# Kernel tuning notes

Hardware: AMD Instinct MI355X
Metric: run time of the kernel (lower is better)

Reference implementation:

```python
import jax, jax.numpy as jnp
import numpy as np

D_MODEL = 1024
NUM_HEADS = 16
DEPTH = D_MODEL // NUM_HEADS
B, S = 4, 2048


def setup_inputs() -> dict:
    key = jax.random.key(0)
    ks = jax.random.split(key, 13)
    sd = 1.0 / np.sqrt(D_MODEL)
    inp = {
        "q_in": jax.random.normal(ks[0], (B, S, D_MODEL), jnp.float32),
        "k_in": jax.random.normal(ks[1], (B, S, D_MODEL), jnp.float32),
        "v_in": jax.random.normal(ks[2], (B, S, D_MODEL), jnp.float32),
        # binary padding/causal-style mask: 1 = masked position
        "m_in": (jax.random.uniform(ks[3], (B, 1, S, S)) < 0.1).astype(jnp.float32),
        "Wq": jax.random.normal(ks[4], (D_MODEL, D_MODEL), jnp.float32) * sd,
        "bq": jax.random.normal(ks[5], (D_MODEL,), jnp.float32) * 0.01,
        "Wk": jax.random.normal(ks[6], (D_MODEL, D_MODEL), jnp.float32) * sd,
        "bk": jax.random.normal(ks[7], (D_MODEL,), jnp.float32) * 0.01,
        "Wv": jax.random.normal(ks[8], (D_MODEL, D_MODEL), jnp.float32) * sd,
        "bv": jax.random.normal(ks[9], (D_MODEL,), jnp.float32) * 0.01,
        "Wo": jax.random.normal(ks[10], (D_MODEL, D_MODEL), jnp.float32) * sd,
        "bo": jax.random.normal(ks[11], (D_MODEL,), jnp.float32) * 0.01,
    }
    return inp


def _split(t):
    # [B,S,D] -> [B,H,S,depth]
    b, s, _ = t.shape
    return t.reshape(b, s, NUM_HEADS, DEPTH).transpose(0, 2, 1, 3)


def reference(q_in, k_in, v_in, m_in, Wq, bq, Wk, bk, Wv, bv, Wo, bo):
    # torch Linear: x @ W^T + b
    q = _split(q_in @ Wq.T + bq)
    k = _split(k_in @ Wk.T + bk)
    v = _split(v_in @ Wv.T + bv)
    scale = jnp.sqrt(jnp.asarray(DEPTH, jnp.float32))
    scores = jnp.einsum("bhqd,bhkd->bhqk", q, k) / scale
    scores = scores - m_in * 1e6
    attn = jax.nn.softmax(scores, axis=-1)
    out = jnp.einsum("bhqk,bhkd->bhqd", attn, v)  # [B,H,S,depth]
    out = out.transpose(0, 2, 1, 3).reshape(q_in.shape[0], -1, D_MODEL)
    return out @ Wo.T + bo
```

## Files before the change

kernel.cpp:

```cpp
#include <hip/hip_runtime.h>


typedef __bf16 bf16_t;
typedef __bf16 bf16x4 __attribute__((ext_vector_type(4)));
typedef __bf16 bf16x8 __attribute__((ext_vector_type(8)));
typedef float floatx2 __attribute__((ext_vector_type(2)));
typedef float floatx4 __attribute__((ext_vector_type(4)));
typedef float floatx16 __attribute__((ext_vector_type(16)));

#define DMODEL 1024
#define NHEAD  16
#define DEPTH  64
#define BATCH  4
#define SEQ    2048
#define MROWS  (BATCH * SEQ)

#define QSCALE 0.18033688011112042f

#define GLDS16(gaddr, laddr)                                                   \
  __builtin_amdgcn_global_load_lds(                                            \
      (__attribute__((address_space(1))) void*)(gaddr),                        \
      (__attribute__((address_space(3))) void*)(laddr), 16, 0, 0)

__global__ __launch_bounds__(256) void cvt_weights(
    const float* __restrict__ w0, const float* __restrict__ w1,
    const float* __restrict__ w2, const float* __restrict__ w3,
    bf16_t* __restrict__ out) {
  const int n_per4 = (DMODEL * DMODEL) / 4;
  int idx = blockIdx.x * blockDim.x + threadIdx.x;
  int t = idx / n_per4;
  int e4 = idx - t * n_per4;
  const float* src = (t == 0) ? w0 : (t == 1) ? w1 : (t == 2) ? w2 : w3;
  const float sc = (t == 0) ? QSCALE : 1.0f;
  float4 v = ((const float4*)src)[e4];
  bf16_t* dst = out + (size_t)t * (DMODEL * DMODEL) + (size_t)e4 * 4;
  dst[0] = (bf16_t)(v.x * sc); dst[1] = (bf16_t)(v.y * sc);
  dst[2] = (bf16_t)(v.z * sc); dst[3] = (bf16_t)(v.w * sc);
}

__global__ __launch_bounds__(256) void cvt3(
    const float* __restrict__ q, const float* __restrict__ k,
    const float* __restrict__ v, bf16_t* __restrict__ dst) {
  const size_t n8 = (size_t)MROWS * DMODEL / 8;
  size_t i = (size_t)blockIdx.x * blockDim.x + threadIdx.x;
  int t = (int)(i / n8);
  size_t e = i - (size_t)t * n8;
  const float* src = (t == 0) ? q : (t == 1) ? k : v;
  const float4* s = (const float4*)(src + e * 8);
  float4 f0 = s[0], f1 = s[1];
  bf16x8 o;
  o[0] = (bf16_t)f0.x; o[1] = (bf16_t)f0.y; o[2] = (bf16_t)f0.z; o[3] = (bf16_t)f0.w;
  o[4] = (bf16_t)f1.x; o[5] = (bf16_t)f1.y; o[6] = (bf16_t)f1.z; o[7] = (bf16_t)f1.w;
  *(bf16x8*)(dst + i * 8) = o;
}

__global__ __launch_bounds__(256) void mask_prepack(
    const float* __restrict__ m, unsigned int* __restrict__ M32) {
  __shared__ unsigned short Mb[32][132];
  const int g = blockIdx.x;
  const int b = blockIdx.y;
  const int tid = threadIdx.x;
  const int lane = tid & 63;
  const int w = tid >> 6;

  const float* base = m + ((size_t)b * SEQ + g * 32) * SEQ;

#pragma unroll
  for (int rr = 0; rr < 8; rr++) {
    const int r = w * 8 + rr;
    const float* row = base + (size_t)r * SEQ;
#pragma unroll
    for (int half = 0; half < 2; half++) {
      const int cg = lane + half * 64;
      unsigned int bits = 0;
#pragma unroll
      for (int j4 = 0; j4 < 4; j4++) {
        const float4 v = *(const float4*)(row + cg * 16 + j4 * 4);
        if (v.x == 0.f) bits |= 1u << (j4 * 4 + 0);
        if (v.y == 0.f) bits |= 1u << (j4 * 4 + 1);
        if (v.z == 0.f) bits |= 1u << (j4 * 4 + 2);
        if (v.w == 0.f) bits |= 1u << (j4 * 4 + 3);
      }
      Mb[r][cg] = (unsigned short)bits;
    }
  }
  __syncthreads();

  const int q = lane & 31, hi = lane >> 5;
  unsigned int* dst = M32 + (size_t)(b * 64 + g) * 32 * 64 + lane;
#pragma unroll
  for (int ii = 0; ii < 8; ii++) {
    const int it = ii * 4 + w;
    unsigned int word = 0;
#pragma unroll
    for (int kb = 0; kb < 2; kb++)
#pragma unroll
      for (int c16 = 0; c16 < 2; c16++) {
        const unsigned int byte =
            ((unsigned int)Mb[q][it * 4 + kb * 2 + c16] >> (hi * 8)) & 0xFFu;
        word |= byte << (kb * 16 + c16 * 8);
      }
    dst[it * 64] = word;
  }
}

__global__ __launch_bounds__(256) void gemm_qkv(
    const bf16_t* __restrict__ Abf3, const bf16_t* __restrict__ Wbf,
    const float* __restrict__ bq, const float* __restrict__ bk,
    const float* __restrict__ bv, bf16_t* __restrict__ Qh,
    bf16_t* __restrict__ Kh, bf16_t* __restrict__ Vth) {
  __shared__ __align__(16) bf16_t As[128 * 64];
  __shared__ __align__(16) bf16_t Bs[128 * 64];
  const int K = DMODEL;
  const int tid = threadIdx.x;
  const int lane = tid & 63;
  const int w = tid >> 6;
  const int quad = lane >> 4;
  const int l16 = lane & 15;
  const int wm = w & 1, wn = w >> 1;
  const int z = blockIdx.z;

  const bf16_t* A = Abf3 + (size_t)z * MROWS * DMODEL;
  const bf16_t* Bt = Wbf + (size_t)z * DMODEL * DMODEL;
  const float* bias = (z == 0) ? bq : (z == 1) ? bk : bv;
  const float bias_scale = (z == 0) ? QSCALE : 1.0f;
  bf16_t* Ov = (z == 0) ? Qh : (z == 1) ? Kh : Vth;

  const int lin = blockIdx.x + 8 * blockIdx.y;
  const int c = lin & 7;
  const int j = lin >> 3;
  const int n0 = (j & 7) * 128;
  const int m0 = ((j >> 3) * 8 + c) * 128;

  const int r8l = lane >> 3;
  const int c8l = (lane & 7) ^ r8l;
  const bf16_t* Ag = A + (size_t)(m0 + w * 32 + r8l) * K + c8l * 8;
  const bf16_t* Bg = Bt + (size_t)(n0 + w * 32 + r8l) * K + c8l * 8;
  char* AsB = (char*)As + (w * 32) * 128;
  char* BsB = (char*)Bs + (w * 32) * 128;

  floatx4 acc[4][4] = {};

  for (int kk = 0; kk < K; kk += 64) {
    __syncthreads();
#pragma unroll
    for (int cl = 0; cl < 4; cl++) {
      GLDS16(Ag + kk + (size_t)(cl * 8) * K, AsB + cl * 8 * 128);
      GLDS16(Bg + kk + (size_t)(cl * 8) * K, BsB + cl * 8 * 128);
    }
    __syncthreads();

#pragma unroll
    for (int kk2 = 0; kk2 < 2; kk2++) {
      bf16x8 af[4], bfr[4];
#pragma unroll
      for (int mi = 0; mi < 4; mi++) {
        const char* Arow = (const char*)As + (wm * 64 + mi * 16 + l16) * 128;
        af[mi] = *(const bf16x8*)(Arow + (((kk2 * 4 + quad) ^ (l16 & 7)) * 16));
      }
#pragma unroll
      for (int ni = 0; ni < 4; ni++) {
        const char* Brow = (const char*)Bs + (wn * 64 + ni * 16 + l16) * 128;
        bfr[ni] = *(const bf16x8*)(Brow + (((kk2 * 4 + quad) ^ (l16 & 7)) * 16));
      }
#pragma unroll
      for (int mi = 0; mi < 4; mi++)
#pragma unroll
        for (int ni = 0; ni < 4; ni++)
          acc[mi][ni] = __builtin_amdgcn_mfma_f32_16x16x32_bf16(af[mi], bfr[ni], acc[mi][ni], 0, 0, 0);
    }
  }

#pragma unroll
  for (int ni = 0; ni < 4; ni++) {
    const int col = n0 + wn * 64 + ni * 16 + l16;
    const float bvl = bias_scale * bias[col];
    const int hh = col >> 6, d = col & (DEPTH - 1);
#pragma unroll
    for (int mi = 0; mi < 4; mi++) {
#pragma unroll
      for (int r = 0; r < 4; r++) {
        const int row = m0 + wm * 64 + mi * 16 + quad * 4 + r;
        const float val = acc[mi][ni][r] + bvl;
        const int bb = row >> 11, s = row & (SEQ - 1);
        if (z != 2) {
          Ov[((((size_t)bb * NHEAD + hh) * SEQ + s) << 6) + d] = (bf16_t)val;
        } else {
          Ov[(((size_t)bb * NHEAD + hh) * DEPTH + d) * SEQ + s] = (bf16_t)val;
        }
      }
    }
  }
}

__global__ __launch_bounds__(256) void gemm_wo(
    const bf16_t* __restrict__ A, const bf16_t* __restrict__ Bt,
    const float* __restrict__ bias, float* __restrict__ Ov,
    int M, int N, int K) {
  __shared__ __align__(16) bf16_t As[128 * 64];
  __shared__ __align__(16) bf16_t Bs[128 * 64];
  const int tid = threadIdx.x;
  const int lane = tid & 63;
  const int w = tid >> 6;
  const int quad = lane >> 4;
  const int l16 = lane & 15;
  const int wm = w & 1, wn = w >> 1;

  const int lin = blockIdx.x + 8 * blockIdx.y;
  const int c = lin & 7;
  const int j = lin >> 3;
  const int n0 = (j & 7) * 128;
  const int m0 = ((j >> 3) * 8 + c) * 128;

  const int r8l = lane >> 3;
  const int c8l = (lane & 7) ^ r8l;
  const bf16_t* Ag = A + (size_t)(m0 + w * 32 + r8l) * K + c8l * 8;
  const bf16_t* Bg = Bt + (size_t)(n0 + w * 32 + r8l) * K + c8l * 8;
  char* AsB = (char*)As + (w * 32) * 128;
  char* BsB = (char*)Bs + (w * 32) * 128;

  floatx4 acc[4][4] = {};

  for (int kk = 0; kk < K; kk += 64) {
    __syncthreads();
#pragma unroll
    for (int cl = 0; cl < 4; cl++) {
      GLDS16(Ag + kk + (size_t)(cl * 8) * K, AsB + cl * 8 * 128);
      GLDS16(Bg + kk + (size_t)(cl * 8) * K, BsB + cl * 8 * 128);
    }
    __syncthreads();

#pragma unroll
    for (int kk2 = 0; kk2 < 2; kk2++) {
      bf16x8 af[4], bfr[4];
#pragma unroll
      for (int mi = 0; mi < 4; mi++) {
        const char* Arow = (const char*)As + (wm * 64 + mi * 16 + l16) * 128;
        af[mi] = *(const bf16x8*)(Arow + (((kk2 * 4 + quad) ^ (l16 & 7)) * 16));
      }
#pragma unroll
      for (int ni = 0; ni < 4; ni++) {
        const char* Brow = (const char*)Bs + (wn * 64 + ni * 16 + l16) * 128;
        bfr[ni] = *(const bf16x8*)(Brow + (((kk2 * 4 + quad) ^ (l16 & 7)) * 16));
      }
#pragma unroll
      for (int mi = 0; mi < 4; mi++)
#pragma unroll
        for (int ni = 0; ni < 4; ni++)
          acc[mi][ni] = __builtin_amdgcn_mfma_f32_16x16x32_bf16(af[mi], bfr[ni], acc[mi][ni], 0, 0, 0);
    }
  }

#pragma unroll
  for (int ni = 0; ni < 4; ni++) {
    const int col = n0 + wn * 64 + ni * 16 + l16;
    const float bv = bias[col];
#pragma unroll
    for (int mi = 0; mi < 4; mi++)
#pragma unroll
      for (int r = 0; r < 4; r++) {
        const int row = m0 + wm * 64 + mi * 16 + quad * 4 + r;
        Ov[(size_t)row * N + col] = acc[mi][ni][r] + bv;
      }
  }
}

__global__ __launch_bounds__(256, 4) void attn_kernel(
    const bf16_t* __restrict__ Qh, const bf16_t* __restrict__ Kh,
    const bf16_t* __restrict__ Vt, const unsigned int* __restrict__ M32,
    bf16_t* __restrict__ O) {
  const int lane = threadIdx.x & 63;
  const int w = __builtin_amdgcn_readfirstlane(threadIdx.x >> 6);
  const int l31 = lane & 31;
  const int hi = lane >> 5;

  const int lin = blockIdx.x + 16 * blockIdx.y + 256 * blockIdx.z;
  const int x8 = lin & 7;
  const int kk = lin >> 3;
  const int qt = kk & 15;
  const int bh = ((kk >> 4) << 3) | x8;
  const int h = bh & 15;
  const int b = bh >> 4;
  const int q0 = qt * 128;

  const bf16_t* Qb = Qh + ((size_t)b * NHEAD + h) * SEQ * DEPTH;
  const bf16_t* Kb = Kh + ((size_t)b * NHEAD + h) * SEQ * DEPTH;
  const bf16_t* Vb = Vt + ((size_t)b * NHEAD + h) * DEPTH * SEQ;
  const unsigned int* Mw =
      M32 + ((size_t)b * 64 + (qt * 4 + w)) * 32 * 64 + lane;

  __shared__ __align__(16) bf16_t Ksm[64 * 64];
  __shared__ __align__(16) bf16_t Vsm[64 * 64];
  __shared__ float Lsm[4][32];

  const int r8 = lane >> 3;
  const int c8 = (lane & 7) ^ r8;
  const int i1 = w * 16 + r8;
  const int i2 = i1 + 8;
  const int lo1 = i1 & 31, lo2 = i2 & 31;
  const int s1 = (i1 & 32) | ((lo1 & ~12) | ((lo1 & 4) << 1) | ((lo1 & 8) >> 1));
  const int s2 = (i2 & 32) | ((lo2 & ~12) | ((lo2 & 4) << 1) | ((lo2 & 8) >> 1));
  const bf16_t* Kg1 = Kb + (size_t)s1 * DEPTH + c8 * 8;
  const bf16_t* Kg2 = Kb + (size_t)s2 * DEPTH + c8 * 8;
  const bf16_t* Vg  = Vb + (size_t)(w * 16 + r8) * SEQ + c8 * 8;
  const int woff = (w * 16) * 128;

  bf16x8 aq[4];
  {
    const bf16_t* qp = Qb + (size_t)(q0 + w * 32 + l31) * DEPTH + hi * 8;
#pragma unroll
    for (int t = 0; t < 4; t++) aq[t] = *(const bf16x8*)(qp + t * 16);
  }

  floatx16 acco[2] = {};
  floatx2 l2 = {0.f, 0.f};
  const int kxor = l31 & 7;

  for (int it = 0; it < SEQ / 64; ++it) {
    const int sk = it * 64;
    const unsigned int mword = Mw[it * 64];
    __syncthreads();
    {
      char* KsB = (char*)Ksm + woff;
      char* VsB = (char*)Vsm + woff;
      GLDS16(Kg1 + (size_t)sk * DEPTH, KsB);
      GLDS16(Kg2 + (size_t)sk * DEPTH, KsB + 8 * 128);
      GLDS16(Vg + sk, VsB);
      GLDS16(Vg + sk + (size_t)8 * SEQ, VsB + 8 * 128);
    }
    __syncthreads();

#pragma unroll
    for (int kb = 0; kb < 2; kb++) {
      floatx16 s = {};
      const char* Krow = (const char*)Ksm + (kb * 32 + l31) * 128;
#pragma unroll
      for (int t = 0; t < 4; t++) {
        bf16x8 kf = *(const bf16x8*)(Krow + (((2 * t + hi) ^ kxor) * 16));
        s = __builtin_amdgcn_mfma_f32_32x32x16_bf16(kf, aq[t], s, 0, 0, 0);
      }
      float pv[16];
#pragma unroll
      for (int r = 0; r < 16; r++) {
        float e = __builtin_amdgcn_exp2f(s[r]);
        const int km = __builtin_amdgcn_sbfe((int)mword, kb * 16 + r, 1);
        pv[r] = __int_as_float(__float_as_int(e) & km);
      }
#pragma unroll
      for (int r = 0; r < 8; r++)
        l2 += (floatx2){pv[2 * r], pv[2 * r + 1]};
#pragma unroll
      for (int mh = 0; mh < 2; mh++) {
        bf16x8 pa;
#pragma unroll
        for (int j2 = 0; j2 < 8; j2++) pa[j2] = (bf16_t)pv[mh * 8 + j2];
        const int m = kb * 2 + mh;
#pragma unroll
        for (int n = 0; n < 2; n++) {
          const char* Vrow = (const char*)Vsm + (n * 32 + l31) * 128;
          bf16x8 vf = *(const bf16x8*)(Vrow + (((2 * m + hi) ^ kxor) * 16));
          acco[n] = __builtin_amdgcn_mfma_f32_32x32x16_bf16(pa, vf, acco[n], 0, 0, 0);
        }
      }
    }
  }

  float lsum = l2.x + l2.y;
  float tot = lsum + __shfl_xor(lsum, 32);
  if (lane < 32) Lsm[w][l31] = __frcp_rn(tot);
  __syncthreads();

#pragma unroll
  for (int r = 0; r < 16; r++) {
    const int qr = (r & 3) + 8 * (r >> 2) + 4 * hi;
    const float inv = Lsm[w][qr];
    const size_t srow = (size_t)q0 + w * 32 + qr;
#pragma unroll
    for (int n = 0; n < 2; n++) {
      const int d = h * DEPTH + n * 32 + l31;
      O[((size_t)b * SEQ + srow) * DMODEL + d] = (bf16_t)(acco[n][r] * inv);
    }
  }
}

extern "C" void kernel_launch(void* const* d_in, const int* in_sizes, int n_in,
                              void* d_out, int out_size, void* d_ws, size_t ws_size,
                              hipStream_t stream) {
  const float* q_in = (const float*)d_in[0];
  const float* k_in = (const float*)d_in[1];
  const float* v_in = (const float*)d_in[2];
  const float* m_in = (const float*)d_in[3];
  const float* Wq = (const float*)d_in[4];
  const float* bq = (const float*)d_in[5];
  const float* Wk = (const float*)d_in[6];
  const float* bk = (const float*)d_in[7];
  const float* Wv = (const float*)d_in[8];
  const float* bv = (const float*)d_in[9];
  const float* Wo = (const float*)d_in[10];
  const float* bo = (const float*)d_in[11];

  char* ws = (char*)d_ws;
  const size_t MB = 1024 * 1024;
  bf16_t* wbf  = (bf16_t*)ws;
  bf16_t* Abf3 = (bf16_t*)(ws + 8 * MB);
  bf16_t* Obuf = (bf16_t*)(ws + 8 * MB);
  bf16_t* Qh   = (bf16_t*)(ws + 56 * MB);
  bf16_t* Kh   = (bf16_t*)(ws + 72 * MB);
  bf16_t* Vth  = (bf16_t*)(ws + 88 * MB);
  unsigned int* M32 = (unsigned int*)(ws + 104 * MB);

  cvt_weights<<<(4 * (DMODEL * DMODEL / 4)) / 256, 256, 0, stream>>>(
      Wq, Wk, Wv, Wo, wbf);
  cvt3<<<(3 * (MROWS * DMODEL / 8)) / 256, 256, 0, stream>>>(
      q_in, k_in, v_in, Abf3);

  dim3 gm(64, BATCH);
  mask_prepack<<<gm, 256, 0, stream>>>(m_in, M32);

  dim3 gqkv(8, 64, 3);
  gemm_qkv<<<gqkv, 256, 0, stream>>>(Abf3, wbf, bq, bk, bv, Qh, Kh, Vth);

  dim3 ga(SEQ / 128, NHEAD, BATCH);
  attn_kernel<<<ga, 256, 0, stream>>>(Qh, Kh, Vth, M32, Obuf);

  dim3 gg(8, 64);
  gemm_wo<<<gg, 256, 0, stream>>>(
      Obuf, wbf + 3 * (size_t)DMODEL * DMODEL, bo, (float*)d_out,
      MROWS, DMODEL, DMODEL);
}
```

Baseline: 406.9 us.

## Merge prep kernels into one launch and halve attention block size

Folds the weight conversion, activation conversion and mask prepack into a single `prep` launch that dispatches on block index, removing two kernel launches and the gaps between them. Separately, the attention kernel moves from 256-thread blocks covering 128 queries to 128-thread blocks covering 64 queries. Each wave now loads twice as many K/V rows into shared memory. This doubles the grid to 2048 blocks for better load balance and occupancy, but every K/V tile is loaded from global memory twice as often per query.

```diff
diff --git a/kernel.cpp b/kernel.cpp
--- a/kernel.cpp
+++ b/kernel.cpp
@@ -22,85 +22,84 @@
       (__attribute__((address_space(1))) void*)(gaddr),                        \
       (__attribute__((address_space(3))) void*)(laddr), 16, 0, 0)
 
-__global__ __launch_bounds__(256) void cvt_weights(
+__global__ __launch_bounds__(256) void prep(
     const float* __restrict__ w0, const float* __restrict__ w1,
     const float* __restrict__ w2, const float* __restrict__ w3,
-    bf16_t* __restrict__ out) {
-  const int n_per4 = (DMODEL * DMODEL) / 4;
-  int idx = blockIdx.x * blockDim.x + threadIdx.x;
-  int t = idx / n_per4;
-  int e4 = idx - t * n_per4;
-  const float* src = (t == 0) ? w0 : (t == 1) ? w1 : (t == 2) ? w2 : w3;
-  const float sc = (t == 0) ? QSCALE : 1.0f;
-  float4 v = ((const float4*)src)[e4];
-  bf16_t* dst = out + (size_t)t * (DMODEL * DMODEL) + (size_t)e4 * 4;
-  dst[0] = (bf16_t)(v.x * sc); dst[1] = (bf16_t)(v.y * sc);
-  dst[2] = (bf16_t)(v.z * sc); dst[3] = (bf16_t)(v.w * sc);
-}
-
-__global__ __launch_bounds__(256) void cvt3(
-    const float* __restrict__ q, const float* __restrict__ k,
-    const float* __restrict__ v, bf16_t* __restrict__ dst) {
-  const size_t n8 = (size_t)MROWS * DMODEL / 8;
-  size_t i = (size_t)blockIdx.x * blockDim.x + threadIdx.x;
-  int t = (int)(i / n8);
-  size_t e = i - (size_t)t * n8;
-  const float* src = (t == 0) ? q : (t == 1) ? k : v;
-  const float4* s = (const float4*)(src + e * 8);
-  float4 f0 = s[0], f1 = s[1];
-  bf16x8 o;
-  o[0] = (bf16_t)f0.x; o[1] = (bf16_t)f0.y; o[2] = (bf16_t)f0.z; o[3] = (bf16_t)f0.w;
-  o[4] = (bf16_t)f1.x; o[5] = (bf16_t)f1.y; o[6] = (bf16_t)f1.z; o[7] = (bf16_t)f1.w;
-  *(bf16x8*)(dst + i * 8) = o;
-}
-
-__global__ __launch_bounds__(256) void mask_prepack(
+    bf16_t* __restrict__ wout,
+    const float* __restrict__ qin, const float* __restrict__ kin,
+    const float* __restrict__ vin, bf16_t* __restrict__ adst,
     const float* __restrict__ m, unsigned int* __restrict__ M32) {
-  __shared__ unsigned short Mb[32][132];
-  const int g = blockIdx.x;
-  const int b = blockIdx.y;
-  const int tid = threadIdx.x;
-  const int lane = tid & 63;
-  const int w = tid >> 6;
-
-  const float* base = m + ((size_t)b * SEQ + g * 32) * SEQ;
-
-#pragma unroll
-  for (int rr = 0; rr < 8; rr++) {
-    const int r = w * 8 + rr;
-    const float* row = base + (size_t)r * SEQ;
-#pragma unroll
-    for (int half = 0; half < 2; half++) {
-      const int cg = lane + half * 64;
-      unsigned int bits = 0;
-#pragma unroll
-      for (int j4 = 0; j4 < 4; j4++) {
-        const float4 v = *(const float4*)(row + cg * 16 + j4 * 4);
-        if (v.x == 0.f) bits |= 1u << (j4 * 4 + 0);
-        if (v.y == 0.f) bits |= 1u << (j4 * 4 + 1);
-        if (v.z == 0.f) bits |= 1u << (j4 * 4 + 2);
-        if (v.w == 0.f) bits |= 1u << (j4 * 4 + 3);
-      }
-      Mb[r][cg] = (unsigned short)bits;
-    }
-  }
-  __syncthreads();
-
-  const int q = lane & 31, hi = lane >> 5;
-  unsigned int* dst = M32 + (size_t)(b * 64 + g) * 32 * 64 + lane;
-#pragma unroll
-  for (int ii = 0; ii < 8; ii++) {
-    const int it = ii * 4 + w;
-    unsigned int word = 0;
-#pragma unroll
-    for (int kb = 0; kb < 2; kb++)
-#pragma unroll
-      for (int c16 = 0; c16 < 2; c16++) {
-        const unsigned int byte =
-            ((unsigned int)Mb[q][it * 4 + kb * 2 + c16] >> (hi * 8)) & 0xFFu;
-        word |= byte << (kb * 16 + c16 * 8);
-      }
-    dst[it * 64] = word;
+  const int bid = blockIdx.x;
+  if (bid < 4096) {
+    const int n_per4 = (DMODEL * DMODEL) / 4;
+    int idx = bid * 256 + threadIdx.x;
+    int t = idx / n_per4;
+    int e4 = idx - t * n_per4;
+    const float* src = (t == 0) ? w0 : (t == 1) ? w1 : (t == 2) ? w2 : w3;
+    const float sc = (t == 0) ? QSCALE : 1.0f;
+    float4 v = ((const float4*)src)[e4];
+    bf16_t* dst = wout + (size_t)t * (DMODEL * DMODEL) + (size_t)e4 * 4;
+    dst[0] = (bf16_t)(v.x * sc); dst[1] = (bf16_t)(v.y * sc);
+    dst[2] = (bf16_t)(v.z * sc); dst[3] = (bf16_t)(v.w * sc);
+  } else if (bid < 16384) {
+    const size_t n8 = (size_t)MROWS * DMODEL / 8;
+    size_t i = (size_t)(bid - 4096) * 256 + threadIdx.x;
+    int t = (int)(i / n8);
+    size_t e = i - (size_t)t * n8;
+    const float* src = (t == 0) ? qin : (t == 1) ? kin : vin;
+    const float4* s = (const float4*)(src + e * 8);
+    float4 f0 = s[0], f1 = s[1];
+    bf16x8 o;
+    o[0] = (bf16_t)f0.x; o[1] = (bf16_t)f0.y; o[2] = (bf16_t)f0.z; o[3] = (bf16_t)f0.w;
+    o[4] = (bf16_t)f1.x; o[5] = (bf16_t)f1.y; o[6] = (bf16_t)f1.z; o[7] = (bf16_t)f1.w;
+    *(bf16x8*)(adst + i * 8) = o;
+  } else {
+    __shared__ unsigned short Mb[32][132];
+    const int r = bid - 16384;
+    const int g = r & 63;
+    const int b = r >> 6;
+    const int tid = threadIdx.x;
+    const int lane = tid & 63;
+    const int w = tid >> 6;
+
+    const float* base = m + ((size_t)b * SEQ + g * 32) * SEQ;
+#pragma unroll
+    for (int rr = 0; rr < 8; rr++) {
+      const int rw = w * 8 + rr;
+      const float* row = base + (size_t)rw * SEQ;
+#pragma unroll
+      for (int half = 0; half < 2; half++) {
+        const int cg = lane + half * 64;
+        unsigned int bits = 0;
+#pragma unroll
+        for (int j4 = 0; j4 < 4; j4++) {
+          const float4 v = *(const float4*)(row + cg * 16 + j4 * 4);
+          if (v.x == 0.f) bits |= 1u << (j4 * 4 + 0);
+          if (v.y == 0.f) bits |= 1u << (j4 * 4 + 1);
+          if (v.z == 0.f) bits |= 1u << (j4 * 4 + 2);
+          if (v.w == 0.f) bits |= 1u << (j4 * 4 + 3);
+        }
+        Mb[rw][cg] = (unsigned short)bits;
+      }
+    }
+    __syncthreads();
+
+    const int q = lane & 31, hi = lane >> 5;
+    unsigned int* dst = M32 + (size_t)(b * 64 + g) * 32 * 64 + lane;
+#pragma unroll
+    for (int ii = 0; ii < 8; ii++) {
+      const int it = ii * 4 + w;
+      unsigned int word = 0;
+#pragma unroll
+      for (int kb = 0; kb < 2; kb++)
+#pragma unroll
+        for (int c16 = 0; c16 < 2; c16++) {
+          const unsigned int byte =
+              ((unsigned int)Mb[q][it * 4 + kb * 2 + c16] >> (hi * 8)) & 0xFFu;
+          word |= byte << (kb * 16 + c16 * 8);
+        }
+      dst[it * 64] = word;
+    }
   }
 }
 
@@ -265,7 +264,7 @@
   }
 }
 
-__global__ __launch_bounds__(256, 4) void attn_kernel(
+__global__ __launch_bounds__(128, 4) void attn_kernel(
     const bf16_t* __restrict__ Qh, const bf16_t* __restrict__ Kh,
     const bf16_t* __restrict__ Vt, const unsigned int* __restrict__ M32,
     bf16_t* __restrict__ O) {
@@ -274,36 +273,38 @@
   const int l31 = lane & 31;
   const int hi = lane >> 5;
 
-  const int lin = blockIdx.x + 16 * blockIdx.y + 256 * blockIdx.z;
+  const int lin = blockIdx.x + 32 * blockIdx.y + 512 * blockIdx.z;
   const int x8 = lin & 7;
   const int kk = lin >> 3;
-  const int qt = kk & 15;
-  const int bh = ((kk >> 4) << 3) | x8;
+  const int qt = kk & 31;
+  const int bh = ((kk >> 5) << 3) | x8;
   const int h = bh & 15;
   const int b = bh >> 4;
-  const int q0 = qt * 128;
+  const int q0 = qt * 64;
 
   const bf16_t* Qb = Qh + ((size_t)b * NHEAD + h) * SEQ * DEPTH;
   const bf16_t* Kb = Kh + ((size_t)b * NHEAD + h) * SEQ * DEPTH;
   const bf16_t* Vb = Vt + ((size_t)b * NHEAD + h) * DEPTH * SEQ;
   const unsigned int* Mw =
-      M32 + ((size_t)b * 64 + (qt * 4 + w)) * 32 * 64 + lane;
+      M32 + ((size_t)b * 64 + (qt * 2 + w)) * 32 * 64 + lane;
 
   __shared__ __align__(16) bf16_t Ksm[64 * 64];
   __shared__ __align__(16) bf16_t Vsm[64 * 64];
-  __shared__ float Lsm[4][32];
+  __shared__ float Lsm[2][32];
 
   const int r8 = lane >> 3;
   const int c8 = (lane & 7) ^ r8;
-  const int i1 = w * 16 + r8;
-  const int i2 = i1 + 8;
-  const int lo1 = i1 & 31, lo2 = i2 & 31;
-  const int s1 = (i1 & 32) | ((lo1 & ~12) | ((lo1 & 4) << 1) | ((lo1 & 8) >> 1));
-  const int s2 = (i2 & 32) | ((lo2 & ~12) | ((lo2 & 4) << 1) | ((lo2 & 8) >> 1));
-  const bf16_t* Kg1 = Kb + (size_t)s1 * DEPTH + c8 * 8;
-  const bf16_t* Kg2 = Kb + (size_t)s2 * DEPTH + c8 * 8;
-  const bf16_t* Vg  = Vb + (size_t)(w * 16 + r8) * SEQ + c8 * 8;
-  const int woff = (w * 16) * 128;
+  const bf16_t* Kg[4];
+#pragma unroll
+  for (int cl = 0; cl < 4; cl++) {
+    const int i = w * 32 + cl * 8 + r8;
+    const int lo = i & 31;
+    const int s = (i & 32) | ((lo & ~12) | ((lo & 4) << 1) | ((lo & 8) >> 1));
+    Kg[cl] = Kb + (size_t)s * DEPTH + c8 * 8;
+  }
+  const bf16_t* Vg = Vb + (size_t)(w * 32 + r8) * SEQ + c8 * 8;
+  char* KsB = (char*)Ksm + (w * 32) * 128;
+  char* VsB = (char*)Vsm + (w * 32) * 128;
 
   bf16x8 aq[4];
   {
@@ -320,14 +321,12 @@
     const int sk = it * 64;
     const unsigned int mword = Mw[it * 64];
     __syncthreads();
-    {
-      char* KsB = (char*)Ksm + woff;
-      char* VsB = (char*)Vsm + woff;
-      GLDS16(Kg1 + (size_t)sk * DEPTH, KsB);
-      GLDS16(Kg2 + (size_t)sk * DEPTH, KsB + 8 * 128);
-      GLDS16(Vg + sk, VsB);
-      GLDS16(Vg + sk + (size_t)8 * SEQ, VsB + 8 * 128);
-    }
+#pragma unroll
+    for (int cl = 0; cl < 4; cl++)
+      GLDS16(Kg[cl] + (size_t)sk * DEPTH, KsB + cl * 8 * 128);
+#pragma unroll
+    for (int cl = 0; cl < 4; cl++)
+      GLDS16(Vg + sk + (size_t)(cl * 8) * SEQ, VsB + cl * 8 * 128);
     __syncthreads();
 
 #pragma unroll
@@ -409,19 +408,14 @@
   bf16_t* Vth  = (bf16_t*)(ws + 88 * MB);
   unsigned int* M32 = (unsigned int*)(ws + 104 * MB);
 
-  cvt_weights<<<(4 * (DMODEL * DMODEL / 4)) / 256, 256, 0, stream>>>(
-      Wq, Wk, Wv, Wo, wbf);
-  cvt3<<<(3 * (MROWS * DMODEL / 8)) / 256, 256, 0, stream>>>(
-      q_in, k_in, v_in, Abf3);
-
-  dim3 gm(64, BATCH);
-  mask_prepack<<<gm, 256, 0, stream>>>(m_in, M32);
+  prep<<<16640, 256, 0, stream>>>(Wq, Wk, Wv, Wo, wbf,
+                                  q_in, k_in, v_in, Abf3, m_in, M32);
 
   dim3 gqkv(8, 64, 3);
   gemm_qkv<<<gqkv, 256, 0, stream>>>(Abf3, wbf, bq, bk, bv, Qh, Kh, Vth);
 
-  dim3 ga(SEQ / 128, NHEAD, BATCH);
-  attn_kernel<<<ga, 256, 0, stream>>>(Qh, Kh, Vth, M32, Obuf);
+  dim3 ga(32, NHEAD, BATCH);
+  attn_kernel<<<ga, 128, 0, stream>>>(Qh, Kh, Vth, M32, Obuf);
 
   dim3 gg(8, 64);
   gemm_wo<<<gg, 256, 0, stream>>>(
```

Measured after the change: 419.8 us. 3.2% more time.
